# Kernel optimization log

Hardware: AMD Instinct MI355X
Metric: run time of the kernel (lower is better)

Reference implementation:

```python
import jax, jax.numpy as jnp
import numpy as np

B, N, E, EH, IB, DF, HID, P, TOPK, NE = 16, 978, 512, 512, 64, 2304, 512, 8, 50, 50000
SKIP = 0.2          # args.graph_skip_conn
NEG_INF = -1e20     # markoff value for non-top-k entries before softmax
LN_EPS = 1e-5


def setup_inputs() -> dict:
    key = jax.random.key(0)
    ks = jax.random.split(key, 20)
    g = lambda i, shape, s=0.05: jax.random.normal(ks[i], shape, dtype=jnp.float32) * s
    return dict(
        x1=jax.random.normal(ks[0], (B, N), dtype=jnp.float32),
        drug1=jax.random.normal(ks[1], (B, DF), dtype=jnp.float32),
        drug2=jax.random.normal(ks[2], (B, DF), dtype=jnp.float32),
        eps=jax.random.normal(ks[3], (B, IB), dtype=jnp.float32),
        edge_index=jax.random.randint(ks[4], (2, NE), 0, N),
        gate_W=g(5, (1, E)), gate_b=jnp.zeros((E,), jnp.float32),
        emb=g(6, (N, E), 1.0),
        encW1=g(7, (E, EH)), encb1=jnp.zeros((EH,), jnp.float32),
        encW2=g(8, (EH, 2 * IB)), encb2=jnp.zeros((2 * IB,), jnp.float32),
        netW1=g(9, (DF, E)), netb1=jnp.zeros((E,), jnp.float32),
        netW2=g(10, (E, 2 * IB)), netb2=jnp.zeros((2 * IB,), jnp.float32),
        ln_g=jnp.ones((2 * IB,), jnp.float32), ln_b=jnp.zeros((2 * IB,), jnp.float32),
        feat_mask=g(11, (4 * IB,), 1.0),
        W_sims=g(12, (P, 4 * IB, HID)),
        gcnW1=g(13, (2 * IB, HID)), gcnb1=jnp.zeros((HID,), jnp.float32),
        gcnW2=g(14, (HID, 2 * IB)), gcnb2=jnp.zeros((2 * IB,), jnp.float32),
        decW1=g(15, (IB, EH)), decb1=jnp.zeros((EH,), jnp.float32),
        bn_g=jnp.ones((EH,), jnp.float32), bn_b=jnp.zeros((EH,), jnp.float32),
        decW2=g(16, (EH, N)), decb2=jnp.zeros((N,), jnp.float32),
    )


def _forward(x1, drug1, drug2, eps, edge_index,
             gate_W, gate_b, emb, encW1, encb1, encW2, encb2,
             netW1, netb1, netW2, netb2, ln_g, ln_b,
             feat_mask, W_sims, gcnW1, gcnb1, gcnW2, gcnb2,
             decW1, decb1, bn_g, bn_b, decW2, decb2):
    # --- Encoder_x1: per-gene gated embedding -> MLP -> [B,N,2*IB] ---
    gate = jax.nn.sigmoid(x1[..., None] @ gate_W + gate_b)          # [B,N,E]
    h = gate * emb[None]                                            # [B,N,E]
    h = jax.nn.gelu(h @ encW1 + encb1, approximate=False)
    H = h @ encW2 + encb2                                           # [B,N,128]

    # --- drug feature net: Linear-ReLU-Linear-LayerNorm -> [B,128] ---
    def drug_embed(d):
        t = jax.nn.relu(d @ netW1 + netb1)
        t = t @ netW2 + netb2
        mu = t.mean(-1, keepdims=True)
        var = t.var(-1, keepdims=True)
        return (t - mu) * jax.lax.rsqrt(var + LN_EPS) * ln_g + ln_b

    D1 = drug_embed(drug1)
    D2 = drug_embed(drug2)
    fus1 = jnp.concatenate([H, jnp.broadcast_to(D1[:, None, :], (B, N, 2 * IB))], -1)  # [B,N,256]
    fus2 = jnp.concatenate([H, jnp.broadcast_to(D2[:, None, :], (B, N, 2 * IB))], -1)

    # --- init adjacency from edge_index (to_dense_adj), shared across batch ---
    init_adj = jnp.zeros((N, N), jnp.float32).at[edge_index[0], edge_index[1]].set(1.0)

    # --- attention-metric graph learner with feature denoise + kNN sparsify ---
    def learn_adj(fus):
        feats = fus * jax.nn.sigmoid(feat_mask)                      # feature mask
        hp = jax.nn.relu(jnp.einsum('bnd,pdh->bpnh', feats, W_sims)) # [B,P,N,HID]
        att = jnp.einsum('bpnh,bpmh->bnm', hp, hp) / P               # [B,N,N] (mean over perspectives)

        def sparsify(a):  # per-sample kNN mask + row softmax
            vals, idx = jax.lax.top_k(a, TOPK)
            out = jnp.full_like(a, NEG_INF).at[jnp.arange(N)[:, None], idx].set(vals)
            return jax.nn.softmax(out, axis=-1)

        adj = jax.vmap(sparsify)(att)
        return SKIP * init_adj[None] + (1.0 - SKIP) * adj

    adj1 = learn_adj(fus1)
    adj2 = learn_adj(fus2)

    # --- 2-layer GCN on learned graph (symmetric norm, self loops, edge weights) ---
    eye = jnp.eye(N, dtype=jnp.float32)

    def gcn_layer(x, adj, W, b):
        ahat = adj + eye[None]
        deg = ahat.sum(-2)                                           # in-degree by target (PyG flow)
        dinv = jax.lax.rsqrt(deg)
        norm = ahat * dinv[:, :, None] * dinv[:, None, :]            # [B,N,N]
        return jnp.einsum('bji,bjf->bif', norm, x @ W) + b

    t = jax.nn.relu(gcn_layer(H, adj1, gcnW1, gcnb1))
    node = gcn_layer(t, adj1, gcnW2, gcnb2)                          # [B,N,128]

    # --- global mean pool + VIB reparametrization ---
    gemb = node.mean(1)                                              # [B,128]
    mu = gemb[:, :IB]
    std = jax.nn.softplus(gemb[:, IB:] - IB)
    z = mu + eps * std                                               # [B,64]

    # --- decoder_x2: Linear-BatchNorm-ReLU-Linear-ReLU ---
    d = z @ decW1 + decb1
    bm = d.mean(0)
    bv = d.var(0)
    d = (d - bm) * jax.lax.rsqrt(bv + LN_EPS) * bn_g + bn_b
    d = jax.nn.relu(d)
    x2_pred = jax.nn.relu(d @ decW2 + decb2)                         # [B,N]
    return x2_pred, adj2, mu, std


def reference(x1, drug1, drug2, eps, edge_index,
              gate_W, gate_b, emb, encW1, encb1, encW2, encb2,
              netW1, netb1, netW2, netb2, ln_g, ln_b,
              feat_mask, W_sims, gcnW1, gcnb1, gcnW2, gcnb2,
              decW1, decb1, bn_g, bn_b, decW2, decb2):
    return _forward(x1, drug1, drug2, eps, edge_index,
                    gate_W, gate_b, emb, encW1, encb1, encW2, encb2,
                    netW1, netb1, netW2, netb2, ln_g, ln_b,
                    feat_mask, W_sims, gcnW1, gcnb1, gcnW2, gcnb2,
                    decW1, decb1, bn_g, bn_b, decW2, decb2)
```

## Files before the change

### kernel.cpp

```cpp
#include <hip/hip_runtime.h>
#include <cmath>

namespace {

constexpr int B = 16;
constexpr int N = 978;
constexpr int M = B * N;
constexpr int IB2 = 128;
constexpr int KATT = 4096;
constexpr int KCH = 1024;
constexpr int NCH = KATT / KCH;
constexpr int DF = 2304;
constexpr int TOPKK = 50;
constexpr int NEDGE = 50000;
constexpr int CANDMAX = 64;
constexpr int WST = 120;
constexpr int JSPLIT = 489;

typedef __attribute__((ext_vector_type(8))) short bf16x8;
typedef __attribute__((ext_vector_type(4))) float f32x4;

__device__ __forceinline__ float geluf(float x) {
  return 0.5f * x * (1.f + erff(x * 0.7071067811865476f));
}
__device__ __forceinline__ float sigm(float x) { return 1.f / (1.f + expf(-x)); }
__device__ __forceinline__ double sigm64(double x) { return 1.0 / (1.0 + exp(-x)); }

__device__ __forceinline__ unsigned short f2bf(float f) {
  union { float f; unsigned u; } x; x.f = f;
  unsigned r = (x.u + 0x7FFFu + ((x.u >> 16) & 1u)) >> 16;
  return (unsigned short)r;
}
__device__ __forceinline__ float bf2f(unsigned short s) {
  union { float f; unsigned u; } x; x.u = ((unsigned)s) << 16; return x.f;
}

__global__ void k_wt(const float* __restrict__ wsims, const float* __restrict__ fm,
                     unsigned short* __restrict__ wth, unsigned short* __restrict__ wtl) {
  int t = blockIdx.x * 256 + threadIdx.x;
  int n = t >> 8, k = t & 255;
  int p = n >> 9, h = n & 511;
  double v = (double)wsims[(size_t)p * 131072 + (size_t)k * 512 + h] * sigm64((double)fm[k]);
  float vf = (float)v;
  unsigned short hi = f2bf(vf);
  wth[t] = hi;
  wtl[t] = f2bf(vf - bf2f(hi));
}

__global__ void k_fus(const float* __restrict__ Hb, const float* __restrict__ DD,
                      unsigned short* __restrict__ fh, unsigned short* __restrict__ fl) {
  int t = blockIdx.x * 256 + threadIdx.x;
  int k = t & 255;
  int row = t >> 8;
  int b = row / N;
  float v = (k < 128) ? Hb[(size_t)row * 128 + k] : DD[(size_t)b * 128 + (k - 128)];
  unsigned short hi = f2bf(v);
  fh[t] = hi;
  fl[t] = f2bf(v - bf2f(hi));
}

__global__ void k_gate_emb(const float* __restrict__ x1, const float* __restrict__ gW,
                           const float* __restrict__ gb, const float* __restrict__ emb,
                           float* __restrict__ A) {
  size_t t = (size_t)blockIdx.x * 256 + threadIdx.x;
  int e = (int)(t & 511);
  size_t bn = t >> 9;
  int n = (int)(bn % N);
  float g = sigm(x1[bn] * gW[e] + gb[e]);
  A[t] = g * emb[(size_t)n * 512 + e];
}

__global__ void k_zero(float* __restrict__ p, int n) {
  int t = blockIdx.x * 256 + threadIdx.x;
  if (t < n) p[t] = 0.f;
}

__global__ void k_scatter(const int* __restrict__ ei, float* __restrict__ adj) {
  int t = blockIdx.x * 256 + threadIdx.x;
  if (t < NEDGE) {
    int r = ei[t], c = ei[NEDGE + t];
    adj[(size_t)r * N + c] = 1.f;
  }
}

template <int ACT, bool HASBIAS>
__global__ __launch_bounds__(256) void k_gemm(const float* __restrict__ A,
                                              const float* __restrict__ W, const float* __restrict__ bias,
                                              float* __restrict__ C,
                                              int Mm, int K, int Nc, int ldw) {
  __shared__ float As[16][132];
  __shared__ float Ws[16][132];
  const int tid = threadIdx.x;
  const int m0 = blockIdx.x * 128;
  const int n0 = blockIdx.y * 128;
  const int ty = tid >> 4, tx = tid & 15;
  float acc[8][8];
#pragma unroll
  for (int i = 0; i < 8; i++)
#pragma unroll
    for (int j = 0; j < 8; j++) acc[i][j] = 0.f;

  for (int k0 = 0; k0 < K; k0 += 16) {
#pragma unroll
    for (int l = 0; l < 2; l++) {
      int idx4 = tid + l * 256;
      int r = idx4 >> 2, c4 = idx4 & 3;
      int row = m0 + r;
      float4 v = make_float4(0.f, 0.f, 0.f, 0.f);
      if (row < Mm) v = *reinterpret_cast<const float4*>(&A[(size_t)row * K + k0 + c4 * 4]);
      As[c4 * 4 + 0][r] = v.x;
      As[c4 * 4 + 1][r] = v.y;
      As[c4 * 4 + 2][r] = v.z;
      As[c4 * 4 + 3][r] = v.w;
    }
#pragma unroll
    for (int l = 0; l < 2; l++) {
      int idx4 = tid + l * 256;
      int r = idx4 >> 5, c4 = idx4 & 31;
      float4 v = *reinterpret_cast<const float4*>(&W[(size_t)(k0 + r) * ldw + n0 + c4 * 4]);
      *reinterpret_cast<float4*>(&Ws[r][c4 * 4]) = v;
    }
    __syncthreads();
#pragma unroll
    for (int k = 0; k < 16; k++) {
      float a[8], bb[8];
      *reinterpret_cast<float4*>(&a[0]) = *reinterpret_cast<const float4*>(&As[k][ty * 8]);
      *reinterpret_cast<float4*>(&a[4]) = *reinterpret_cast<const float4*>(&As[k][ty * 8 + 4]);
      *reinterpret_cast<float4*>(&bb[0]) = *reinterpret_cast<const float4*>(&Ws[k][tx * 8]);
      *reinterpret_cast<float4*>(&bb[4]) = *reinterpret_cast<const float4*>(&Ws[k][tx * 8 + 4]);
#pragma unroll
      for (int i = 0; i < 8; i++)
#pragma unroll
        for (int j = 0; j < 8; j++) acc[i][j] = fmaf(a[i], bb[j], acc[i][j]);
    }
    __syncthreads();
  }
#pragma unroll
  for (int i = 0; i < 8; i++) {
    int row = m0 + ty * 8 + i;
    if (row >= Mm) continue;
#pragma unroll
    for (int j4 = 0; j4 < 2; j4++) {
      float4 v;
      float* vv = reinterpret_cast<float*>(&v);
#pragma unroll
      for (int j = 0; j < 4; j++) {
        float x = acc[i][j4 * 4 + j];
        if (HASBIAS) x += bias[n0 + tx * 8 + j4 * 4 + j];
        if (ACT == 1) x = geluf(x);
        if (ACT == 2) x = fmaxf(x, 0.f);
        vv[j] = x;
      }
      *reinterpret_cast<float4*>(&C[(size_t)row * Nc + n0 + tx * 8 + j4 * 4]) = v;
    }
  }
}

__device__ __forceinline__ void stage_tile(const unsigned short* __restrict__ gbase, int grow0,
                                           int rowmax, int k0, int ldk, char* lds, int tid) {
#pragma unroll
  for (int it = 0; it < 2; it++) {
    int r = (tid >> 2) + it * 64;
    int c8 = tid & 3;
    int gr = grow0 + r;
    uint4 v = make_uint4(0u, 0u, 0u, 0u);
    if (gr < rowmax) v = *reinterpret_cast<const uint4*>(&gbase[(size_t)gr * ldk + k0 + c8 * 8]);
    int off = (r * 64 + c8 * 16) ^ ((r & 7) << 4);
    *reinterpret_cast<uint4*>(lds + off) = v;
  }
}

__device__ __forceinline__ bf16x8 frag(const char* lds, int r, int k8) {
  int off = (r * 64 + k8 * 16) ^ ((r & 7) << 4);
  return *reinterpret_cast<const bf16x8*>(lds + off);
}

__global__ __launch_bounds__(256) void k_hp_mma(const unsigned short* __restrict__ FH,
                                                const unsigned short* __restrict__ FL,
                                                const unsigned short* __restrict__ WTHc,
                                                const unsigned short* __restrict__ WTLc,
                                                float* __restrict__ CH) {
  __shared__ __align__(16) char Ah[8192];
  __shared__ __align__(16) char Al[8192];
  __shared__ __align__(16) char Bh[8192];
  __shared__ __align__(16) char Bl[8192];
  const int m0 = blockIdx.x * 128;
  const int n0 = blockIdx.y * 128;
  const int tid = threadIdx.x;
  const int wave = tid >> 6, lane = tid & 63;
  f32x4 acc[2][8];
#pragma unroll
  for (int i = 0; i < 2; i++)
#pragma unroll
    for (int j = 0; j < 8; j++) acc[i][j] = (f32x4){0.f, 0.f, 0.f, 0.f};

  for (int k0 = 0; k0 < 256; k0 += 32) {
    stage_tile(FH, m0, M, k0, 256, Ah, tid);
    stage_tile(FL, m0, M, k0, 256, Al, tid);
    stage_tile(WTHc, n0, KCH, k0, 256, Bh, tid);
    stage_tile(WTLc, n0, KCH, k0, 256, Bl, tid);
    __syncthreads();
    bf16x8 ah[2], al[2];
#pragma unroll
    for (int rf = 0; rf < 2; rf++) {
      int r = wave * 32 + rf * 16 + (lane & 15);
      ah[rf] = frag(Ah, r, lane >> 4);
      al[rf] = frag(Al, r, lane >> 4);
    }
#pragma unroll
    for (int cf = 0; cf < 8; cf++) {
      int rB = cf * 16 + (lane & 15);
      bf16x8 bh = frag(Bh, rB, lane >> 4);
      bf16x8 bl = frag(Bl, rB, lane >> 4);
#pragma unroll
      for (int rf = 0; rf < 2; rf++) {
        acc[rf][cf] = __builtin_amdgcn_mfma_f32_16x16x32_bf16(ah[rf], bh, acc[rf][cf], 0, 0, 0);
        acc[rf][cf] = __builtin_amdgcn_mfma_f32_16x16x32_bf16(ah[rf], bl, acc[rf][cf], 0, 0, 0);
        acc[rf][cf] = __builtin_amdgcn_mfma_f32_16x16x32_bf16(al[rf], bh, acc[rf][cf], 0, 0, 0);
      }
    }
    __syncthreads();
  }
#pragma unroll
  for (int rf = 0; rf < 2; rf++)
#pragma unroll
    for (int cf = 0; cf < 8; cf++)
#pragma unroll
      for (int r4 = 0; r4 < 4; r4++) {
        int row = m0 + wave * 32 + rf * 16 + ((lane >> 4) << 2) + r4;
        int col = n0 + cf * 16 + (lane & 15);
        if (row < M) CH[(size_t)row * KCH + col] = fmaxf(acc[rf][cf][r4], 0.f);
      }
}

__global__ __launch_bounds__(256) void k_mu(const float* __restrict__ CH, float* __restrict__ MU) {
  __shared__ double red[8][33];
  int b = blockIdx.y, jg = blockIdx.x;
  int jloc = threadIdx.x & 31, s = threadIdx.x >> 5;
  int j = jg * 32 + jloc;
  const float* p = CH + (size_t)b * N * KCH + j;
  double acc = 0.0;
  for (int n = s; n < N; n += 8) acc += (double)p[(size_t)n * KCH];
  red[s][jloc] = acc;
  __syncthreads();
  if (s == 0) {
    double t = 0.0;
#pragma unroll
    for (int k = 0; k < 8; k++) t += red[k][jloc];
    MU[b * KCH + j] = (float)(t * (1.0 / (double)N));
  }
}

__global__ __launch_bounds__(256) void k_centerq(const float* __restrict__ CH,
                                                 const float* __restrict__ MU,
                                                 unsigned short* __restrict__ CHB,
                                                 double* __restrict__ qv) {
  int r = blockIdx.x * 4 + (threadIdx.x >> 6);
  int lane = threadIdx.x & 63;
  int b = r / N;
  const float* row = CH + (size_t)r * KCH;
  const float* mu = MU + (size_t)b * KCH;
  double q = 0.0;
#pragma unroll
  for (int jp = 0; jp < 2; jp++) {
    int j0 = lane * 8 + jp * 512;
    float4 v0 = *reinterpret_cast<const float4*>(&row[j0]);
    float4 v1 = *reinterpret_cast<const float4*>(&row[j0 + 4]);
    float4 m0 = *reinterpret_cast<const float4*>(&mu[j0]);
    float4 m1 = *reinterpret_cast<const float4*>(&mu[j0 + 4]);
    unsigned short cb[8];
    cb[0] = f2bf(v0.x - m0.x); cb[1] = f2bf(v0.y - m0.y);
    cb[2] = f2bf(v0.z - m0.z); cb[3] = f2bf(v0.w - m0.w);
    cb[4] = f2bf(v1.x - m1.x); cb[5] = f2bf(v1.y - m1.y);
    cb[6] = f2bf(v1.z - m1.z); cb[7] = f2bf(v1.w - m1.w);
    *reinterpret_cast<uint4*>(&CHB[(size_t)r * KCH + j0]) = *reinterpret_cast<uint4*>(cb);
    q += (double)m0.x * v0.x + (double)m0.y * v0.y + (double)m0.z * v0.z + (double)m0.w * v0.w
       + (double)m1.x * v1.x + (double)m1.y * v1.y + (double)m1.z * v1.z + (double)m1.w * v1.w;
  }
  for (int off = 32; off > 0; off >>= 1) q += __shfl_down(q, off);
  if (lane == 0) qv[r] += q;
}

template <bool ACC>
__global__ __launch_bounds__(256) void k_syrk_mma(const unsigned short* __restrict__ CHB,
                                                  float* __restrict__ ATT) {
  __shared__ __align__(16) char At[8192];
  __shared__ __align__(16) char Bt[8192];
  const int T = 8;
  int pr = blockIdx.x;
  int ti = 0, rem = pr;
  while (rem >= T - ti) { rem -= T - ti; ti++; }
  int tj = ti + rem;
  int b = blockIdx.y;
  const unsigned short* base = CHB + (size_t)b * N * KCH;
  const int tid = threadIdx.x;
  const int wave = tid >> 6, lane = tid & 63;
  f32x4 acc[2][8];
#pragma unroll
  for (int i = 0; i < 2; i++)
#pragma unroll
    for (int j = 0; j < 8; j++) acc[i][j] = (f32x4){0.f, 0.f, 0.f, 0.f};

  for (int k0 = 0; k0 < KCH; k0 += 32) {
    stage_tile(base, ti * 128, N, k0, KCH, At, tid);
    stage_tile(base, tj * 128, N, k0, KCH, Bt, tid);
    __syncthreads();
    bf16x8 af[2];
#pragma unroll
    for (int rf = 0; rf < 2; rf++)
      af[rf] = frag(At, wave * 32 + rf * 16 + (lane & 15), lane >> 4);
#pragma unroll
    for (int cf = 0; cf < 8; cf++) {
      bf16x8 bf_ = frag(Bt, cf * 16 + (lane & 15), lane >> 4);
#pragma unroll
      for (int rf = 0; rf < 2; rf++)
        acc[rf][cf] = __builtin_amdgcn_mfma_f32_16x16x32_bf16(af[rf], bf_, acc[rf][cf], 0, 0, 0);
    }
    __syncthreads();
  }
  float* att = ATT + (size_t)b * N * N;
#pragma unroll
  for (int rf = 0; rf < 2; rf++)
#pragma unroll
    for (int cf = 0; cf < 8; cf++)
#pragma unroll
      for (int r4 = 0; r4 < 4; r4++) {
        int row = ti * 128 + wave * 32 + rf * 16 + ((lane >> 4) << 2) + r4;
        int col = tj * 128 + cf * 16 + (lane & 15);
        if (row < N && col < N) {
          float v = acc[rf][cf][r4];
          if (ACC) {
            att[(size_t)row * N + col] += v;
            if (ti != tj) att[(size_t)col * N + row] += v;
          } else {
            att[(size_t)row * N + col] = v;
            if (ti != tj) att[(size_t)col * N + row] = v;
          }
        }
      }
}

__global__ __launch_bounds__(256) void k_topk(float* __restrict__ ATT, const double* __restrict__ qv,
                                              const float* __restrict__ INITA,
                                              int* __restrict__ fcnt, int* __restrict__ frow,
                                              int* __restrict__ fcw, int* __restrict__ fidx,
                                              float* __restrict__ fv32) {
  int row = blockIdx.x;
  int n = row % N;
  int b = row / N;
  float* arow = ATT + (size_t)row * N;
  __shared__ unsigned long long keys[1024];
  __shared__ float outr[N];
  __shared__ float sred;
  __shared__ int s_slot, s_cw;
  int tid = threadIdx.x;
  double qn = qv[row];
  unsigned long long kreg[4];
#pragma unroll
  for (int c = 0; c < 4; c++) {
    int i = tid + 256 * c;
    unsigned long long kk = 0xFFFFFFFFFFFFFFFFull;
    if (i < N) {
      float sv = (float)((double)arow[i] + qv[(size_t)b * N + i] - qn);
      unsigned u = __float_as_uint(sv);
      u ^= (u >> 31) ? 0xFFFFFFFFu : 0x80000000u;
      kk = ((unsigned long long)(~u) << 32) | (unsigned)i;
    }
    kreg[c] = kk;
  }
  for (int ksz = 2; ksz <= 1024; ksz <<= 1) {
    for (int j = ksz >> 1; j > 0; j >>= 1) {
      if (j <= 32) {
#pragma unroll
        for (int c = 0; c < 4; c++) {
          int e = tid + 256 * c;
          unsigned long long pk = __shfl_xor(kreg[c], j);
          bool takemin = (((e & j) == 0) == ((e & ksz) == 0));
          unsigned long long mn = kreg[c] < pk ? kreg[c] : pk;
          unsigned long long mx = kreg[c] < pk ? pk : kreg[c];
          kreg[c] = takemin ? mn : mx;
        }
      } else if (j >= 256) {
        int sw = j >> 8;
#pragma unroll
        for (int c = 0; c < 4; c++) {
          if ((c & sw) == 0) {
            int e = tid + 256 * c;
            bool up = (e & ksz) == 0;
            unsigned long long a = kreg[c], b2 = kreg[c | sw];
            if ((a > b2) == up) { kreg[c] = b2; kreg[c | sw] = a; }
          }
        }
      } else {
#pragma unroll
        for (int c = 0; c < 4; c++) keys[tid + 256 * c] = kreg[c];
        __syncthreads();
#pragma unroll
        for (int c = 0; c < 4; c++) {
          int e = tid + 256 * c;
          unsigned long long pk = keys[e ^ j];
          bool takemin = (((e & j) == 0) == ((e & ksz) == 0));
          unsigned long long mn = kreg[c] < pk ? kreg[c] : pk;
          unsigned long long mx = kreg[c] < pk ? pk : kreg[c];
          kreg[c] = takemin ? mn : mx;
        }
        __syncthreads();
      }
    }
  }
#pragma unroll
  for (int c = 0; c < 4; c++) keys[tid + 256 * c] = kreg[c];
  __syncthreads();
  auto dec = [](unsigned long long kk) {
    unsigned y = ~(unsigned)(kk >> 32);
    unsigned u = (y & 0x80000000u) ? (y ^ 0x80000000u) : ~y;
    return __uint_as_float(u);
  };

  float v49 = dec(keys[49]);
  float v50v = dec(keys[50]);
  float FLAGW = 8e-3f + 2e-5f * fabsf(v49);
  bool flag = (v50v >= v49 - FLAGW);
  if (flag) {
    if (tid == 0) {
      int cin = 0;
      for (int r = 0; r < 50; r++)
        if (dec(keys[r]) > v49 + FLAGW) cin++;
      int rhi = 50;
      while (rhi < 113) {
        float vv = dec(keys[rhi + 1]);
        if (vv >= v49 - FLAGW) rhi++; else break;
      }
      int w = rhi - cin + 1;
      if (w > CANDMAX) w = CANDMAX;
      if (cin + w < 50) w = 50 - cin;
      int slot = atomicAdd(fcnt, 1);
      frow[slot] = row;
      fcw[slot] = cin | (w << 8);
      s_slot = slot;
      s_cw = cin | (w << 8);
    }
    __syncthreads();
    int slot = s_slot;
    int tot = (s_cw & 255) + (s_cw >> 8);
    for (int r = tid; r < tot; r += 256) {
      unsigned long long kk = keys[r];
      fidx[(size_t)slot * WST + r] = (int)(unsigned)(kk & 0xFFFFFFFFull);
      fv32[(size_t)slot * WST + r] = dec(kk);
    }
    __syncthreads();
  }

  float vmax = dec(keys[0]);
  float e = 0.f;
  int myidx = 0;
  if (tid < TOPKK) {
    unsigned long long kk = keys[tid];
    myidx = (int)(unsigned)(kk & 0xFFFFFFFFull);
    e = expf((dec(kk) - vmax) * 0.125f);
  }
  float s = e;
  for (int off = 32; off > 0; off >>= 1) s += __shfl_down(s, off);
  if (tid == 0) sred = s;
  for (int m2 = tid; m2 < N; m2 += 256) outr[m2] = 0.2f * INITA[(size_t)n * N + m2];
  __syncthreads();
  if (tid < TOPKK) outr[myidx] = 0.2f * INITA[(size_t)n * N + myidx] + 0.8f * (e / sred);
  __syncthreads();
  for (int m2 = tid; m2 < N; m2 += 256) arow[m2] = outr[m2];
}

__global__ __launch_bounds__(256) void k_fixup(float* __restrict__ ATT, const float* __restrict__ INITA,
                                               const int* __restrict__ fcnt, const int* __restrict__ frow,
                                               const int* __restrict__ fcw, const int* __restrict__ fidx,
                                               const float* __restrict__ fv32) {
  __shared__ double wts[56];
  __shared__ int mm[56];
  __shared__ int s_tot;
  int tid = threadIdx.x;
  int cnt = *fcnt;
  for (int slot = blockIdx.x; slot < cnt; slot += gridDim.x) {
    int row = frow[slot];
    int cw = fcw[slot];
    int cin = cw & 255, w = cw >> 8;
    int n = row % N;
    __syncthreads();
    if (tid == 0) {
      int need = 50 - cin;
      if (need > w) need = w;
      double cv[CANDMAX]; int cm[CANDMAX]; float cs[CANDMAX];
      for (int c = 0; c < w; c++) {
        float sv = fv32[(size_t)slot * WST + cin + c];
        cv[c] = (double)sv * 0.125;
        cm[c] = fidx[(size_t)slot * WST + cin + c];
        cs[c] = sv;
      }
      int ord[CANDMAX];
      for (int c = 0; c < w; c++) ord[c] = c;
      for (int a2 = 0; a2 < w; a2++) {
        int best = a2;
        for (int c2 = a2 + 1; c2 < w; c2++) {
          int i1 = ord[c2], i0 = ord[best];
          if (cv[i1] > cv[i0] || (cv[i1] == cv[i0] && cm[i1] < cm[i0])) best = c2;
        }
        int tswap = ord[a2]; ord[a2] = ord[best]; ord[best] = tswap;
      }
      double b_in = cv[ord[need - 1]];
      double b_out = (need < w) ? cv[ord[need]] : -1e300;
      const double DATT = 1e-3;
      double fac[56];
      int tot = 0;
      for (int r = 0; r < cin; r++) {
        wts[tot] = (double)fv32[(size_t)slot * WST + r];
        mm[tot] = fidx[(size_t)slot * WST + r];
        fac[tot++] = 1.0;
      }
      if (need == w || b_in - b_out > DATT) {
        for (int t3 = 0; t3 < need; t3++) {
          wts[tot] = (double)cs[ord[t3]];
          mm[tot] = cm[ord[t3]];
          fac[tot++] = 1.0;
        }
      } else {
        int gs = 0;
        while (gs < w && cv[ord[gs]] > b_in + DATT) gs++;
        int ge = w - 1;
        while (ge >= 0 && cv[ord[ge]] < b_out - DATT) ge--;
        double mid = 0.5 * (b_in + b_out);
        while (ge - gs + 1 > 3) {
          if (cv[ord[gs]] - mid >= mid - cv[ord[ge]]) gs++;
          else ge--;
        }
        int fullc = gs;
        int gcount = ge - gs + 1;
        int gneed = need - fullc;
        if (gneed < 0) gneed = 0;
        if (gneed > gcount) gneed = gcount;
        double frac = (gcount > 0) ? (double)gneed / (double)gcount : 0.0;
        for (int t3 = 0; t3 < fullc; t3++) {
          wts[tot] = (double)cs[ord[t3]];
          mm[tot] = cm[ord[t3]];
          fac[tot++] = 1.0;
        }
        for (int t3 = gs; t3 <= ge; t3++) {
          wts[tot] = (double)cs[ord[t3]];
          mm[tot] = cm[ord[t3]];
          fac[tot++] = frac;
        }
      }
      double vmax = -1e300;
      for (int r = 0; r < tot; r++)
        if (fac[r] > 0.0 && wts[r] > vmax) vmax = wts[r];
      double S = 0.0;
      for (int r = 0; r < tot; r++) {
        double e = fac[r] * exp((wts[r] - vmax) * 0.125);
        wts[r] = e;
        S += e;
      }
      double inv = 1.0 / S;
      for (int r = 0; r < tot; r++) wts[r] *= inv;
      s_tot = tot;
    }
    __syncthreads();
    int tot = s_tot;
    float* arow = ATT + (size_t)row * N;
    for (int m2 = tid; m2 < N; m2 += 256) arow[m2] = 0.2f * INITA[(size_t)n * N + m2];
    __syncthreads();
    if (tid < tot && wts[tid] > 0.0)
      arow[mm[tid]] = 0.2f * INITA[(size_t)n * N + mm[tid]] + 0.8f * (float)wts[tid];
    __syncthreads();
  }
}

__global__ __launch_bounds__(256) void k_degp(const float* __restrict__ ADJ, float* __restrict__ DPART) {
  int ch = blockIdx.x, b = blockIdx.y;
  int tid = threadIdx.x;
  float reg[4] = {0.f, 0.f, 0.f, 0.f};
  int j0 = ch * 123, j1 = j0 + 123;
  if (j1 > N) j1 = N;
  const float* adj = ADJ + (size_t)b * N * N;
  for (int j = j0; j < j1; j++) {
    const float* rowp = adj + (size_t)j * N;
#pragma unroll
    for (int k = 0; k < 4; k++) {
      int i = tid + 256 * k;
      if (i < N) reg[k] += rowp[i];
    }
  }
  float* dp = DPART + ((size_t)b * 8 + ch) * N;
#pragma unroll
  for (int k = 0; k < 4; k++) {
    int i = tid + 256 * k;
    if (i < N) dp[i] = reg[k];
  }
}
__global__ void k_degf(const float* __restrict__ DPART, float* __restrict__ DINV) {
  int t = blockIdx.x * 256 + threadIdx.x;
  if (t >= M) return;
  int b = t / N, i = t - b * N;
  float s = 1.f;
#pragma unroll
  for (int c = 0; c < 8; c++) s += DPART[((size_t)b * 8 + c) * N + i];
  DINV[t] = rsqrtf(s);
}

__global__ __launch_bounds__(256) void k_spmmp(const float* __restrict__ ADJ, const float* __restrict__ DINV,
                                               const float* __restrict__ X, float* __restrict__ PP) {
  __shared__ float As[16][132];
  __shared__ float Ws[16][132];
  const int tid = threadIdx.x;
  const int i0 = blockIdx.x * 128;
  const int b = blockIdx.z >> 1;
  const int half = blockIdx.z & 1;
  const int jstart = half ? JSPLIT : 0;
  const int jend = half ? N : JSPLIT;
  const float* adj = ADJ + (size_t)b * N * N;
  const float* dv = DINV + b * N;
  const float* xb = X + (size_t)b * N * 128;
  const int ty = tid >> 4, tx = tid & 15;
  float acc[8][8];
#pragma unroll
  for (int i = 0; i < 8; i++)
#pragma unroll
    for (int j = 0; j < 8; j++) acc[i][j] = 0.f;

  for (int j0 = jstart; j0 < jend; j0 += 16) {
#pragma unroll
    for (int l = 0; l < 8; l++) {
      int idx = tid + l * 256;
      int r = idx >> 7, c = idx & 127;
      int j = j0 + r, i = i0 + c;
      float v = 0.f;
      if (j < jend && i < N) {
        float dj = dv[j];
        v = adj[(size_t)j * N + i] * dj;
        if (i == j) v += dj;
      }
      As[r][c] = v;
      float w = 0.f;
      if (j < jend) w = xb[(size_t)j * 128 + c];
      Ws[r][c] = w;
    }
    __syncthreads();
#pragma unroll
    for (int k = 0; k < 16; k++) {
      float a[8], bb[8];
      *reinterpret_cast<float4*>(&a[0]) = *reinterpret_cast<const float4*>(&As[k][ty * 8]);
      *reinterpret_cast<float4*>(&a[4]) = *reinterpret_cast<const float4*>(&As[k][ty * 8 + 4]);
      *reinterpret_cast<float4*>(&bb[0]) = *reinterpret_cast<const float4*>(&Ws[k][tx * 8]);
      *reinterpret_cast<float4*>(&bb[4]) = *reinterpret_cast<const float4*>(&Ws[k][tx * 8 + 4]);
#pragma unroll
      for (int i = 0; i < 8; i++)
#pragma unroll
        for (int j = 0; j < 8; j++) acc[i][j] = fmaf(a[i], bb[j], acc[i][j]);
    }
    __syncthreads();
  }
#pragma unroll
  for (int i = 0; i < 8; i++) {
    int row = i0 + ty * 8 + i;
    if (row >= N) continue;
#pragma unroll
    for (int j4 = 0; j4 < 2; j4++) {
      float4 v;
      float* vv = reinterpret_cast<float*>(&v);
#pragma unroll
      for (int j = 0; j < 4; j++) vv[j] = acc[i][j4 * 4 + j];
      *reinterpret_cast<float4*>(&PP[(((size_t)half * M) + (size_t)b * N + row) * 128 +
                                     tx * 8 + j4 * 4]) = v;
    }
  }
}

template <bool HASBIAS>
__global__ void k_spmmc(const float* __restrict__ PP, const float* __restrict__ DINV,
                        const float* __restrict__ bias, float* __restrict__ OUT) {
  int t = blockIdx.x * 256 + threadIdx.x;
  int row = t >> 7, f = t & 127;
  float v = (PP[t] + PP[(size_t)M * 128 + t]) * DINV[row];
  if (HASBIAS) v += bias[f];
  OUT[t] = v;
}

__global__ __launch_bounds__(256) void k_drug_l1(const float* __restrict__ d1, const float* __restrict__ d2,
                                                 const float* __restrict__ W, const float* __restrict__ bias,
                                                 float* __restrict__ T1) {
  __shared__ float row[DF];
  int blk = blockIdx.x;
  const float* dr = ((blk & 16) ? d2 : d1) + (size_t)(blk & 15) * DF;
  for (int i = threadIdx.x; i < DF; i += 256) row[i] = dr[i];
  __syncthreads();
  for (int e = threadIdx.x; e < 512; e += 256) {
    float s = bias[e];
    for (int k = 0; k < DF; k++) s = fmaf(row[k], W[(size_t)k * 512 + e], s);
    T1[(size_t)blk * 512 + e] = fmaxf(s, 0.f);
  }
}

__global__ __launch_bounds__(128) void k_drug_l2(const float* __restrict__ T1, const float* __restrict__ W,
                                                 const float* __restrict__ bias, const float* __restrict__ lg,
                                                 const float* __restrict__ lb, float* __restrict__ D) {
  __shared__ float row[512];
  __shared__ float red[4];
  int blk = blockIdx.x;
  int e = threadIdx.x;
  for (int i = e; i < 512; i += 128) row[i] = T1[(size_t)blk * 512 + i];
  __syncthreads();
  float s = bias[e];
  for (int k = 0; k < 512; k++) s = fmaf(row[k], W[k * 128 + e], s);
  float t = s;
  for (int off = 32; off > 0; off >>= 1) t += __shfl_down(t, off);
  if ((e & 63) == 0) red[e >> 6] = t;
  __syncthreads();
  float mean = (red[0] + red[1]) * (1.f / 128.f);
  float dd = s - mean;
  float wv = dd * dd;
  for (int off = 32; off > 0; off >>= 1) wv += __shfl_down(wv, off);
  if ((e & 63) == 0) red[2 + (e >> 6)] = wv;
  __syncthreads();
  float var = (red[2] + red[3]) * (1.f / 128.f);
  D[(size_t)blk * 128 + e] = dd * rsqrtf(var + 1e-5f) * lg[e] + lb[e];
}

__global__ void k_gemb(const float* __restrict__ NODE, float* __restrict__ GEMB) {
  int t = blockIdx.x * 256 + threadIdx.x;
  int b = t >> 7, f = t & 127;
  const float* p = NODE + (size_t)b * N * IB2 + f;
  float s = 0.f;
  for (int n2 = 0; n2 < N; n2++) s += p[(size_t)n2 * IB2];
  GEMB[t] = s * (1.f / (float)N);
}

__global__ void k_heads(const float* __restrict__ GEMB, const float* __restrict__ EPS,
                        float* __restrict__ out_mu, float* __restrict__ out_std, float* __restrict__ Z) {
  int t = blockIdx.x * 256 + threadIdx.x;
  int b = t >> 6, q = t & 63;
  float mu = GEMB[b * 128 + q];
  float xs = GEMB[b * 128 + 64 + q] - 64.f;
  float sp = (xs > 20.f) ? xs : log1pf(expf(xs));
  out_mu[t] = mu;
  out_std[t] = sp;
  Z[t] = mu + EPS[t] * sp;
}

__global__ __launch_bounds__(512) void k_dec1(const float* __restrict__ Z, const float* __restrict__ W1,
                                              const float* __restrict__ b1, const float* __restrict__ bg,
                                              const float* __restrict__ bb, float* __restrict__ DEC) {
  int f = threadIdx.x;
  float d[16];
  for (int b = 0; b < 16; b++) {
    float s = b1[f];
    for (int k = 0; k < 64; k++) s = fmaf(Z[b * 64 + k], W1[k * 512 + f], s);
    d[b] = s;
  }
  float m = 0.f;
  for (int b = 0; b < 16; b++) m += d[b];
  m *= (1.f / 16.f);
  float v = 0.f;
  for (int b = 0; b < 16; b++) { float t = d[b] - m; v += t * t; }
  v *= (1.f / 16.f);
  float sc = rsqrtf(v + 1e-5f) * bg[f];
  float sh = bb[f];
  for (int b = 0; b < 16; b++) {
    float x = (d[b] - m) * sc + sh;
    DEC[b * 512 + f] = fmaxf(x, 0.f);
  }
}

__global__ void k_dec2(const float* __restrict__ DEC, const float* __restrict__ W2,
                       const float* __restrict__ b2, float* __restrict__ X2) {
  int t = blockIdx.x * 256 + threadIdx.x;
  if (t >= M) return;
  int b = t / N, n2 = t - b * N;
  float s = b2[n2];
  const float* db = DEC + b * 512;
  for (int f = 0; f < 512; f++) s = fmaf(db[f], W2[(size_t)f * N + n2], s);
  X2[t] = fmaxf(s, 0.f);
}

}

extern "C" void kernel_launch(void* const* d_in, const int* in_sizes, int n_in,
                              void* d_out, int out_size, void* d_ws, size_t ws_size,
                              hipStream_t stream) {
  const float* x1 = (const float*)d_in[0];
  const float* drug1 = (const float*)d_in[1];
  const float* drug2 = (const float*)d_in[2];
  const float* eps = (const float*)d_in[3];
  const int* ei = (const int*)d_in[4];
  const float* gate_W = (const float*)d_in[5];
  const float* gate_b = (const float*)d_in[6];
  const float* emb = (const float*)d_in[7];
  const float* encW1 = (const float*)d_in[8];
  const float* encb1 = (const float*)d_in[9];
  const float* encW2 = (const float*)d_in[10];
  const float* encb2 = (const float*)d_in[11];
  const float* netW1 = (const float*)d_in[12];
  const float* netb1 = (const float*)d_in[13];
  const float* netW2 = (const float*)d_in[14];
  const float* netb2 = (const float*)d_in[15];
  const float* ln_g = (const float*)d_in[16];
  const float* ln_b = (const float*)d_in[17];
  const float* feat_mask = (const float*)d_in[18];
  const float* W_sims = (const float*)d_in[19];
  const float* gcnW1 = (const float*)d_in[20];
  const float* gcnb1 = (const float*)d_in[21];
  const float* gcnW2 = (const float*)d_in[22];
  const float* gcnb2 = (const float*)d_in[23];
  const float* decW1 = (const float*)d_in[24];
  const float* decb1 = (const float*)d_in[25];
  const float* bn_g = (const float*)d_in[26];
  const float* bn_b = (const float*)d_in[27];
  const float* decW2 = (const float*)d_in[28];
  const float* decb2 = (const float*)d_in[29];
  (void)in_sizes; (void)n_in; (void)out_size; (void)ws_size;

  size_t o = 0;
  auto A = [&](size_t bytes) { char* p = (char*)d_ws + o; o += (bytes + 255) & ~(size_t)255; return p; };
  unsigned short* WTH = (unsigned short*)A((size_t)KATT * 256 * 2);
  unsigned short* WTL = (unsigned short*)A((size_t)KATT * 256 * 2);
  char* RBIG = A((size_t)64 * 1024 * 1024);
  float* Hb = (float*)A((size_t)M * 128 * 4);
  float* ADJ1 = (float*)A((size_t)B * N * N * 4);
  float* INITA = (float*)A((size_t)N * N * 4);
  float* T1 = (float*)A(32 * 512 * 4);
  float* Dd32 = (float*)A(32 * 128 * 4);
  float* DINV = (float*)A(M * 4);
  float* DPART = (float*)A((size_t)16 * 8 * N * 4);
  float* GEMB = (float*)A(B * 128 * 4);
  float* Zb = (float*)A(B * 64 * 4);
  float* DEC = (float*)A(B * 512 * 4);
  int* fcnt = (int*)A(256);
  float* MU = (float*)A((size_t)B * KCH * 4);
  double* qv = (double*)A((size_t)M * 8);
  unsigned short* FUSH = (unsigned short*)A((size_t)M * 256 * 2);
  unsigned short* FUSL = (unsigned short*)A((size_t)M * 256 * 2);
  unsigned short* CHB = (unsigned short*)A((size_t)M * KCH * 2);

  float* buf1 = (float*)RBIG;
  float* buf2 = (float*)(RBIG + (size_t)32 * 1024 * 1024);
  float* CH = (float*)RBIG;
  char* FLAGS = RBIG;
  int* frow = (int*)FLAGS;
  int* fcw = (int*)(FLAGS + (size_t)M * 4);
  int* fidx = (int*)(FLAGS + (size_t)2 * M * 4);
  float* fv32 = (float*)(FLAGS + (size_t)2 * M * 4 + (size_t)M * WST * 4);
  float* AGG = (float*)RBIG;
  float* PP = (float*)(RBIG + (size_t)8 * 1024 * 1024);
  float* Tt = (float*)(RBIG + (size_t)32 * 1024 * 1024);
  float* TW2 = (float*)FUSH;
  float* NODE = (float*)FUSL;

  float* out = (float*)d_out;
  float* out_x2 = out;
  float* out_adj2 = out + M;
  float* out_mu = out + M + (size_t)B * N * N;
  float* out_std = out_mu + B * 64;

  k_wt<<<4096, 256, 0, stream>>>(W_sims, feat_mask, WTH, WTL);
  k_gate_emb<<<31296, 256, 0, stream>>>(x1, gate_W, gate_b, emb, buf1);
  k_gemm<1, true><<<dim3(123, 4), 256, 0, stream>>>(buf1, encW1, encb1, buf2, M, 512, 512, 512);
  k_gemm<0, true><<<dim3(123, 1), 256, 0, stream>>>(buf2, encW2, encb2, Hb, M, 512, 128, 128);
  k_drug_l1<<<32, 256, 0, stream>>>(drug1, drug2, netW1, netb1, T1);
  k_drug_l2<<<32, 128, 0, stream>>>(T1, netW2, netb2, ln_g, ln_b, Dd32);
  k_zero<<<(N * N + 255) / 256, 256, 0, stream>>>(INITA, N * N);
  k_scatter<<<(NEDGE + 255) / 256, 256, 0, stream>>>(ei, INITA);

  for (int g = 0; g < 2; g++) {
    float* att = (g == 0) ? ADJ1 : out_adj2;
    const float* DDg = Dd32 + (size_t)g * 16 * 128;
    hipMemsetAsync(fcnt, 0, 4, stream);
    hipMemsetAsync(qv, 0, (size_t)M * 8, stream);
    k_fus<<<15648, 256, 0, stream>>>(Hb, DDg, FUSH, FUSL);
    for (int c = 0; c < NCH; c++) {
      k_hp_mma<<<dim3(123, KCH / 128), 256, 0, stream>>>(FUSH, FUSL, WTH + (size_t)c * KCH * 256,
                                                         WTL + (size_t)c * KCH * 256, CH);
      k_mu<<<dim3(KCH / 32, 16), 256, 0, stream>>>(CH, MU);
      k_centerq<<<M / 4, 256, 0, stream>>>(CH, MU, CHB, qv);
      if (c == 0)
        k_syrk_mma<false><<<dim3(36, 16), 256, 0, stream>>>(CHB, att);
      else
        k_syrk_mma<true><<<dim3(36, 16), 256, 0, stream>>>(CHB, att);
    }
    k_topk<<<M, 256, 0, stream>>>(att, qv, INITA, fcnt, frow, fcw, fidx, fv32);
    k_fixup<<<1024, 256, 0, stream>>>(att, INITA, fcnt, frow, fcw, fidx, fv32);
  }

  k_degp<<<dim3(8, 16), 256, 0, stream>>>(ADJ1, DPART);
  k_degf<<<(M + 255) / 256, 256, 0, stream>>>(DPART, DINV);
  k_spmmp<<<dim3(8, 1, 32), 256, 0, stream>>>(ADJ1, DINV, Hb, PP);
  k_spmmc<false><<<(M * 128) / 256, 256, 0, stream>>>(PP, DINV, nullptr, AGG);
  k_gemm<2, true><<<dim3(123, 4), 256, 0, stream>>>(AGG, gcnW1, gcnb1, Tt, M, 128, 512, 512);
  k_gemm<0, false><<<dim3(123, 1), 256, 0, stream>>>(Tt, gcnW2, nullptr, TW2, M, 512, 128, 128);
  k_spmmp<<<dim3(8, 1, 32), 256, 0, stream>>>(ADJ1, DINV, TW2, PP);
  k_spmmc<true><<<(M * 128) / 256, 256, 0, stream>>>(PP, DINV, gcnb2, NODE);
  k_gemb<<<8, 256, 0, stream>>>(NODE, GEMB);
  k_heads<<<4, 256, 0, stream>>>(GEMB, eps, out_mu, out_std, Zb);
  k_dec1<<<1, 512, 0, stream>>>(Zb, decW1, decb1, bn_g, bn_b, DEC);
  k_dec2<<<(M + 255) / 256, 256, 0, stream>>>(DEC, decW2, decb2, out_x2);
}
```

Before: 3.909 ms.

## Move encoder and GCN dense GEMMs to split-bf16 MFMA kernels

Result: no change. 3.838 ms (-1.8%).

```diff
diff --git a/kernel.cpp b/kernel.cpp
--- a/kernel.cpp
+++ b/kernel.cpp
@@ -47,6 +47,17 @@
   wtl[t] = f2bf(vf - bf2f(hi));
 }
 
+__global__ void k_wtrans(const float* __restrict__ W, unsigned short* __restrict__ TH,
+                         unsigned short* __restrict__ TL, int K, int Nc) {
+  int t = blockIdx.x * 256 + threadIdx.x;
+  if (t >= K * Nc) return;
+  int n = t / K, k = t - n * K;
+  float v = W[(size_t)k * Nc + n];
+  unsigned short hi = f2bf(v);
+  TH[t] = hi;
+  TL[t] = f2bf(v - bf2f(hi));
+}
+
 __global__ void k_fus(const float* __restrict__ Hb, const float* __restrict__ DD,
                       unsigned short* __restrict__ fh, unsigned short* __restrict__ fl) {
   int t = blockIdx.x * 256 + threadIdx.x;
@@ -59,15 +70,18 @@
   fl[t] = f2bf(v - bf2f(hi));
 }
 
-__global__ void k_gate_emb(const float* __restrict__ x1, const float* __restrict__ gW,
-                           const float* __restrict__ gb, const float* __restrict__ emb,
-                           float* __restrict__ A) {
+__global__ void k_gate_emb_bf(const float* __restrict__ x1, const float* __restrict__ gW,
+                              const float* __restrict__ gb, const float* __restrict__ emb,
+                              unsigned short* __restrict__ GH, unsigned short* __restrict__ GL) {
   size_t t = (size_t)blockIdx.x * 256 + threadIdx.x;
   int e = (int)(t & 511);
   size_t bn = t >> 9;
   int n = (int)(bn % N);
   float g = sigm(x1[bn] * gW[e] + gb[e]);
-  A[t] = g * emb[(size_t)n * 512 + e];
+  float v = g * emb[(size_t)n * 512 + e];
+  unsigned short hi = f2bf(v);
+  GH[t] = hi;
+  GL[t] = f2bf(v - bf2f(hi));
 }
 
 __global__ void k_zero(float* __restrict__ p, int n) {
@@ -80,79 +94,6 @@
   if (t < NEDGE) {
     int r = ei[t], c = ei[NEDGE + t];
     adj[(size_t)r * N + c] = 1.f;
-  }
-}
-
-template <int ACT, bool HASBIAS>
-__global__ __launch_bounds__(256) void k_gemm(const float* __restrict__ A,
-                                              const float* __restrict__ W, const float* __restrict__ bias,
-                                              float* __restrict__ C,
-                                              int Mm, int K, int Nc, int ldw) {
-  __shared__ float As[16][132];
-  __shared__ float Ws[16][132];
-  const int tid = threadIdx.x;
-  const int m0 = blockIdx.x * 128;
-  const int n0 = blockIdx.y * 128;
-  const int ty = tid >> 4, tx = tid & 15;
-  float acc[8][8];
-#pragma unroll
-  for (int i = 0; i < 8; i++)
-#pragma unroll
-    for (int j = 0; j < 8; j++) acc[i][j] = 0.f;
-
-  for (int k0 = 0; k0 < K; k0 += 16) {
-#pragma unroll
-    for (int l = 0; l < 2; l++) {
-      int idx4 = tid + l * 256;
-      int r = idx4 >> 2, c4 = idx4 & 3;
-      int row = m0 + r;
-      float4 v = make_float4(0.f, 0.f, 0.f, 0.f);
-      if (row < Mm) v = *reinterpret_cast<const float4*>(&A[(size_t)row * K + k0 + c4 * 4]);
-      As[c4 * 4 + 0][r] = v.x;
-      As[c4 * 4 + 1][r] = v.y;
-      As[c4 * 4 + 2][r] = v.z;
-      As[c4 * 4 + 3][r] = v.w;
-    }
-#pragma unroll
-    for (int l = 0; l < 2; l++) {
-      int idx4 = tid + l * 256;
-      int r = idx4 >> 5, c4 = idx4 & 31;
-      float4 v = *reinterpret_cast<const float4*>(&W[(size_t)(k0 + r) * ldw + n0 + c4 * 4]);
-      *reinterpret_cast<float4*>(&Ws[r][c4 * 4]) = v;
-    }
-    __syncthreads();
-#pragma unroll
-    for (int k = 0; k < 16; k++) {
-      float a[8], bb[8];
-      *reinterpret_cast<float4*>(&a[0]) = *reinterpret_cast<const float4*>(&As[k][ty * 8]);
-      *reinterpret_cast<float4*>(&a[4]) = *reinterpret_cast<const float4*>(&As[k][ty * 8 + 4]);
-      *reinterpret_cast<float4*>(&bb[0]) = *reinterpret_cast<const float4*>(&Ws[k][tx * 8]);
-      *reinterpret_cast<float4*>(&bb[4]) = *reinterpret_cast<const float4*>(&Ws[k][tx * 8 + 4]);
-#pragma unroll
-      for (int i = 0; i < 8; i++)
-#pragma unroll
-        for (int j = 0; j < 8; j++) acc[i][j] = fmaf(a[i], bb[j], acc[i][j]);
-    }
-    __syncthreads();
-  }
-#pragma unroll
-  for (int i = 0; i < 8; i++) {
-    int row = m0 + ty * 8 + i;
-    if (row >= Mm) continue;
-#pragma unroll
-    for (int j4 = 0; j4 < 2; j4++) {
-      float4 v;
-      float* vv = reinterpret_cast<float*>(&v);
-#pragma unroll
-      for (int j = 0; j < 4; j++) {
-        float x = acc[i][j4 * 4 + j];
-        if (HASBIAS) x += bias[n0 + tx * 8 + j4 * 4 + j];
-        if (ACT == 1) x = geluf(x);
-        if (ACT == 2) x = fmaxf(x, 0.f);
-        vv[j] = x;
-      }
-      *reinterpret_cast<float4*>(&C[(size_t)row * Nc + n0 + tx * 8 + j4 * 4]) = v;
-    }
   }
 }
 
@@ -173,6 +114,81 @@
 __device__ __forceinline__ bf16x8 frag(const char* lds, int r, int k8) {
   int off = (r * 64 + k8 * 16) ^ ((r & 7) << 4);
   return *reinterpret_cast<const bf16x8*>(lds + off);
+}
+
+template <int ACT, bool HASBIAS, bool OUTF32, bool OUTBF>
+__global__ __launch_bounds__(256) void k_mgemm(const unsigned short* __restrict__ AH,
+                                               const unsigned short* __restrict__ AL,
+                                               const unsigned short* __restrict__ BTH,
+                                               const unsigned short* __restrict__ BTL,
+                                               const float* __restrict__ bias,
+                                               float* __restrict__ Cf,
+                                               unsigned short* __restrict__ CbH,
+                                               unsigned short* __restrict__ CbL,
+                                               int Mm, int K, int Nc) {
+  __shared__ __align__(16) char Ah[8192];
+  __shared__ __align__(16) char Al[8192];
+  __shared__ __align__(16) char Bh[8192];
+  __shared__ __align__(16) char Bl[8192];
+  const int m0 = blockIdx.x * 128;
+  const int n0 = blockIdx.y * 128;
+  const int tid = threadIdx.x;
+  const int wave = tid >> 6, lane = tid & 63;
+  f32x4 acc[2][8];
+#pragma unroll
+  for (int i = 0; i < 2; i++)
+#pragma unroll
+    for (int j = 0; j < 8; j++) acc[i][j] = (f32x4){0.f, 0.f, 0.f, 0.f};
+
+  for (int k0 = 0; k0 < K; k0 += 32) {
+    stage_tile(AH, m0, Mm, k0, K, Ah, tid);
+    stage_tile(AL, m0, Mm, k0, K, Al, tid);
+    stage_tile(BTH, n0, Nc, k0, K, Bh, tid);
+    stage_tile(BTL, n0, Nc, k0, K, Bl, tid);
+    __syncthreads();
+    bf16x8 ah[2], al[2];
+#pragma unroll
+    for (int rf = 0; rf < 2; rf++) {
+      int r = wave * 32 + rf * 16 + (lane & 15);
+      ah[rf] = frag(Ah, r, lane >> 4);
+      al[rf] = frag(Al, r, lane >> 4);
+    }
+#pragma unroll
+    for (int cf = 0; cf < 8; cf++) {
+      int rB = cf * 16 + (lane & 15);
+      bf16x8 bh = frag(Bh, rB, lane >> 4);
+      bf16x8 bl = frag(Bl, rB, lane >> 4);
+#pragma unroll
+      for (int rf = 0; rf < 2; rf++) {
+        acc[rf][cf] = __builtin_amdgcn_mfma_f32_16x16x32_bf16(ah[rf], bh, acc[rf][cf], 0, 0, 0);
+        acc[rf][cf] = __builtin_amdgcn_mfma_f32_16x16x32_bf16(ah[rf], bl, acc[rf][cf], 0, 0, 0);
+        acc[rf][cf] = __builtin_amdgcn_mfma_f32_16x16x32_bf16(al[rf], bh, acc[rf][cf], 0, 0, 0);
+      }
+    }
+    __syncthreads();
+  }
+#pragma unroll
+  for (int rf = 0; rf < 2; rf++)
+#pragma unroll
+    for (int cf = 0; cf < 8; cf++)
+#pragma unroll
+      for (int r4 = 0; r4 < 4; r4++) {
+        int row = m0 + wave * 32 + rf * 16 + ((lane >> 4) << 2) + r4;
+        int col = n0 + cf * 16 + (lane & 15);
+        if (row < Mm) {
+          float v = acc[rf][cf][r4];
+          if (HASBIAS) v += bias[col];
+          if (ACT == 1) v = geluf(v);
+          if (ACT == 2) v = fmaxf(v, 0.f);
+          size_t idx = (size_t)row * Nc + col;
+          if (OUTF32) Cf[idx] = v;
+          if (OUTBF) {
+            unsigned short hi = f2bf(v);
+            CbH[idx] = hi;
+            CbL[idx] = f2bf(v - bf2f(hi));
+          }
+        }
+      }
 }
 
 __global__ __launch_bounds__(256) void k_hp_mma(const unsigned short* __restrict__ FH,
@@ -671,14 +687,21 @@
   }
 }
 
-template <bool HASBIAS>
+template <bool HASBIAS, bool OUTBF>
 __global__ void k_spmmc(const float* __restrict__ PP, const float* __restrict__ DINV,
-                        const float* __restrict__ bias, float* __restrict__ OUT) {
+                        const float* __restrict__ bias, float* __restrict__ OUT,
+                        unsigned short* __restrict__ OH, unsigned short* __restrict__ OL) {
   int t = blockIdx.x * 256 + threadIdx.x;
   int row = t >> 7, f = t & 127;
   float v = (PP[t] + PP[(size_t)M * 128 + t]) * DINV[row];
   if (HASBIAS) v += bias[f];
-  OUT[t] = v;
+  if (OUTBF) {
+    unsigned short hi = f2bf(v);
+    OH[t] = hi;
+    OL[t] = f2bf(v - bf2f(hi));
+  } else {
+    OUT[t] = v;
+  }
 }
 
 __global__ __launch_bounds__(256) void k_drug_l1(const float* __restrict__ d1, const float* __restrict__ d2,
@@ -835,18 +858,30 @@
   unsigned short* FUSH = (unsigned short*)A((size_t)M * 256 * 2);
   unsigned short* FUSL = (unsigned short*)A((size_t)M * 256 * 2);
   unsigned short* CHB = (unsigned short*)A((size_t)M * KCH * 2);
-
-  float* buf1 = (float*)RBIG;
-  float* buf2 = (float*)(RBIG + (size_t)32 * 1024 * 1024);
+  unsigned short* WE1H = (unsigned short*)A(512 * 512 * 2);
+  unsigned short* WE1L = (unsigned short*)A(512 * 512 * 2);
+  unsigned short* WE2H = (unsigned short*)A(128 * 512 * 2);
+  unsigned short* WE2L = (unsigned short*)A(128 * 512 * 2);
+  unsigned short* WG1H = (unsigned short*)A(512 * 128 * 2);
+  unsigned short* WG1L = (unsigned short*)A(512 * 128 * 2);
+  unsigned short* WG2H = (unsigned short*)A(128 * 512 * 2);
+  unsigned short* WG2L = (unsigned short*)A(128 * 512 * 2);
+
+  unsigned short* GEH = (unsigned short*)RBIG;
+  unsigned short* GEL = (unsigned short*)(RBIG + (size_t)16 * 1024 * 1024);
+  unsigned short* H1H = (unsigned short*)(RBIG + (size_t)32 * 1024 * 1024);
+  unsigned short* H1L = (unsigned short*)(RBIG + (size_t)48 * 1024 * 1024);
   float* CH = (float*)RBIG;
   char* FLAGS = RBIG;
   int* frow = (int*)FLAGS;
   int* fcw = (int*)(FLAGS + (size_t)M * 4);
   int* fidx = (int*)(FLAGS + (size_t)2 * M * 4);
   float* fv32 = (float*)(FLAGS + (size_t)2 * M * 4 + (size_t)M * WST * 4);
-  float* AGG = (float*)RBIG;
+  unsigned short* AGGH = (unsigned short*)RBIG;
+  unsigned short* AGGL = (unsigned short*)(RBIG + (size_t)4 * 1024 * 1024);
   float* PP = (float*)(RBIG + (size_t)8 * 1024 * 1024);
-  float* Tt = (float*)(RBIG + (size_t)32 * 1024 * 1024);
+  unsigned short* TTH = (unsigned short*)(RBIG + (size_t)32 * 1024 * 1024);
+  unsigned short* TTL = (unsigned short*)(RBIG + (size_t)48 * 1024 * 1024);
   float* TW2 = (float*)FUSH;
   float* NODE = (float*)FUSL;
 
@@ -857,9 +892,15 @@
   float* out_std = out_mu + B * 64;
 
   k_wt<<<4096, 256, 0, stream>>>(W_sims, feat_mask, WTH, WTL);
-  k_gate_emb<<<31296, 256, 0, stream>>>(x1, gate_W, gate_b, emb, buf1);
-  k_gemm<1, true><<<dim3(123, 4), 256, 0, stream>>>(buf1, encW1, encb1, buf2, M, 512, 512, 512);
-  k_gemm<0, true><<<dim3(123, 1), 256, 0, stream>>>(buf2, encW2, encb2, Hb, M, 512, 128, 128);
+  k_wtrans<<<1024, 256, 0, stream>>>(encW1, WE1H, WE1L, 512, 512);
+  k_wtrans<<<256, 256, 0, stream>>>(encW2, WE2H, WE2L, 512, 128);
+  k_wtrans<<<256, 256, 0, stream>>>(gcnW1, WG1H, WG1L, 128, 512);
+  k_wtrans<<<256, 256, 0, stream>>>(gcnW2, WG2H, WG2L, 512, 128);
+  k_gate_emb_bf<<<31296, 256, 0, stream>>>(x1, gate_W, gate_b, emb, GEH, GEL);
+  k_mgemm<1, true, false, true><<<dim3(123, 4), 256, 0, stream>>>(
+      GEH, GEL, WE1H, WE1L, encb1, nullptr, H1H, H1L, M, 512, 512);
+  k_mgemm<0, true, true, false><<<dim3(123, 1), 256, 0, stream>>>(
+      H1H, H1L, WE2H, WE2L, encb2, Hb, nullptr, nullptr, M, 512, 128);
   k_drug_l1<<<32, 256, 0, stream>>>(drug1, drug2, netW1, netb1, T1);
   k_drug_l2<<<32, 128, 0, stream>>>(T1, netW2, netb2, ln_g, ln_b, Dd32);
   k_zero<<<(N * N + 255) / 256, 256, 0, stream>>>(INITA, N * N);
@@ -888,11 +929,13 @@
   k_degp<<<dim3(8, 16), 256, 0, stream>>>(ADJ1, DPART);
   k_degf<<<(M + 255) / 256, 256, 0, stream>>>(DPART, DINV);
   k_spmmp<<<dim3(8, 1, 32), 256, 0, stream>>>(ADJ1, DINV, Hb, PP);
-  k_spmmc<false><<<(M * 128) / 256, 256, 0, stream>>>(PP, DINV, nullptr, AGG);
-  k_gemm<2, true><<<dim3(123, 4), 256, 0, stream>>>(AGG, gcnW1, gcnb1, Tt, M, 128, 512, 512);
-  k_gemm<0, false><<<dim3(123, 1), 256, 0, stream>>>(Tt, gcnW2, nullptr, TW2, M, 512, 128, 128);
+  k_spmmc<false, true><<<(M * 128) / 256, 256, 0, stream>>>(PP, DINV, nullptr, nullptr, AGGH, AGGL);
+  k_mgemm<2, true, false, true><<<dim3(123, 4), 256, 0, stream>>>(
+      AGGH, AGGL, WG1H, WG1L, gcnb1, nullptr, TTH, TTL, M, 128, 512);
+  k_mgemm<0, false, true, false><<<dim3(123, 1), 256, 0, stream>>>(
+      TTH, TTL, WG2H, WG2L, nullptr, TW2, nullptr, nullptr, M, 512, 128);
   k_spmmp<<<dim3(8, 1, 32), 256, 0, stream>>>(ADJ1, DINV, TW2, PP);
-  k_spmmc<true><<<(M * 128) / 256, 256, 0, stream>>>(PP, DINV, gcnb2, NODE);
+  k_spmmc<true, false><<<(M * 128) / 256, 256, 0, stream>>>(PP, DINV, gcnb2, NODE, nullptr, nullptr);
   k_gemb<<<8, 256, 0, stream>>>(NODE, GEMB);
   k_heads<<<4, 256, 0, stream>>>(GEMB, eps, out_mu, out_std, Zb);
   k_dec1<<<1, 512, 0, stream>>>(Zb, decW1, decb1, bn_g, bn_b, DEC);
```
